# Kernel optimization log

Measured on AMD Instinct MI355X. Metric: run time of the kernel, lower is better.

Reference implementation:

```python
import jax, jax.numpy as jnp
from jax import lax
import numpy as np

B, F, H, W, D = 256, 64, 64, 64, 256  # batch, features_dim, map H, map W, input_dim
HC = 32  # hidden conv channels


def setup_inputs() -> dict:
    key = jax.random.key(0)
    ks = jax.random.split(key, 10)
    s = 0.02
    return {
        "x": jax.random.normal(ks[0], (B, D), jnp.float32),
        "state": jax.random.normal(ks[1], (B, F, H, W), jnp.float32),
        "index": jax.random.randint(ks[2], (B, 2), 0, H),
        "conv1_w": jax.random.normal(ks[3], (HC, F, 3, 3), jnp.float32) * s,
        "conv1_b": jnp.zeros((HC,), jnp.float32),
        "conv2_w": jax.random.normal(ks[4], (HC, HC, 3, 3), jnp.float32) * s,
        "conv2_b": jnp.zeros((HC,), jnp.float32),
        "conv3_w": jax.random.normal(ks[5], (HC, HC, 3, 3), jnp.float32) * s,
        "conv3_b": jnp.zeros((HC,), jnp.float32),
        "lin_w": jax.random.normal(ks[6], (HC * H * W, F), jnp.float32) * s,
        "lin_b": jnp.zeros((F,), jnp.float32),
        "write_w": jax.random.normal(ks[7], (D + 2 * F, F), jnp.float32) * s,
        "write_b": jnp.zeros((F,), jnp.float32),
    }


def _conv_relu(h, w, b):
    y = lax.conv_general_dilated(h, w, (1, 1), "SAME",
                                 dimension_numbers=("NCHW", "OIHW", "NCHW"))
    return jax.nn.relu(y + b[None, :, None, None])


def reference(x, state, index, conv1_w, conv1_b, conv2_w, conv2_b,
              conv3_w, conv3_b, lin_w, lin_b, write_w, write_b):
    h = _conv_relu(state, conv1_w, conv1_b)
    h = _conv_relu(h, conv2_w, conv2_b)
    h = _conv_relu(h, conv3_w, conv3_b)
    r = jax.nn.relu(h.reshape(B, -1) @ lin_w + lin_b)  # [B, F]
    # write: gather per-batch map cell, single Linear (MLP with no hidden layers)
    bidx = jnp.arange(B)
    m = state[bidx, :, index[:, 0], index[:, 1]]  # [B, F] gather
    w = jnp.concatenate([x, r, m], axis=1) @ write_w + write_b  # [B, F]
    # scatter updated feature vector back into the state map
    new_state = state.at[bidx, :, index[:, 0], index[:, 1]].set(w)
    return jnp.concatenate([r, w], axis=1), new_state
```

## Files before the change

kernel.cpp:

```cpp
#include <hip/hip_runtime.h>
#include <hip/hip_bf16.h>


typedef __attribute__((ext_vector_type(8))) short bf16x8;
typedef __attribute__((ext_vector_type(4))) float f32x4;

__device__ inline unsigned short f2bfu(float f) {
    __hip_bfloat16 h = __float2bfloat16(f);
    return *reinterpret_cast<unsigned short*>(&h);
}

__global__ __launch_bounds__(256)
void repack_w_k(const float* __restrict__ w1, const float* __restrict__ w2,
                const float* __restrict__ w3, __hip_bfloat16* __restrict__ rw)
{
    int idx = blockIdx.x * 256 + threadIdx.x;
    const float* src; int CIN, li;
    if (idx < 18432)      { src = w1; CIN = 64; li = idx; }
    else if (idx < 27648) { src = w2; CIN = 32; li = idx - 18432; }
    else                  { src = w3; CIN = 32; li = idx - 27648; }
    int ci = li & 31;
    int co = (li >> 5) & 31;
    int t2 = li >> 10;
    int ks = t2 % 9;
    int ch = t2 / 9;
    rw[idx] = __float2bfloat16(src[((size_t)(co * CIN + ch * 32 + ci)) * 9 + ks]);
}

template<int CIN, typename TIN>
__global__ __launch_bounds__(256, 2)
void conv_mfma_k(const TIN* __restrict__ in,
                 const __hip_bfloat16* __restrict__ rw,
                 const float* __restrict__ bias,
                 __hip_bfloat16* __restrict__ out)
{
    constexpr int NCH = CIN / 32;
    __shared__ __hip_bfloat16 s_in[18 * 34 * 40];

    const int b    = blockIdx.x;
    const int ty0  = (blockIdx.y >> 1) * 16;
    const int tx0  = (blockIdx.y & 1) * 32;
    const int t    = threadIdx.x;
    const int lane = t & 63;
    const int wv   = t >> 6;
    const int ln   = lane & 15;
    const int lg   = lane >> 4;

    const f32x4 zero4 = {0.f, 0.f, 0.f, 0.f};
    f32x4 acc[8][2];
    #pragma unroll
    for (int p = 0; p < 8; ++p) { acc[p][0] = zero4; acc[p][1] = zero4; }

    int bbase[8];
    #pragma unroll
    for (int p = 0; p < 8; ++p) {
        int gg = wv * 8 + p;
        bbase[p] = (((gg >> 1) * 34) + (gg & 1) * 16 + ln) * 80 + lg * 16;
    }

    for (int ch = 0; ch < NCH; ++ch) {
        bf16x8 wf[9][2];
        #pragma unroll
        for (int ks = 0; ks < 9; ++ks)
            #pragma unroll
            for (int cg = 0; cg < 2; ++cg)
                wf[ks][cg] = *(const bf16x8*)(rw + ((size_t)((ch * 9 + ks) * 32 + cg * 16 + ln)) * 32 + lg * 8);

        if constexpr (sizeof(TIN) == 4) {
            for (int idx = t; idx < 32 * 18 * 34; idx += 256) {
                int lx = idx % 34;
                int r  = idx / 34;
                int ly = r % 18;
                int ci = r / 18;
                int gy = ty0 - 1 + ly, gx = tx0 - 1 + lx;
                float v = 0.f;
                if ((unsigned)gy < 64u && (unsigned)gx < 64u)
                    v = in[(((size_t)b * CIN + ch * 32 + ci) * 64 + gy) * 64 + gx];
                s_in[(ly * 34 + lx) * 40 + ci] = __float2bfloat16(v);
            }
        } else {
            for (int idx = t; idx < 18 * 34 * 4; idx += 256) {
                int c8 = idx & 3, px = idx >> 2;
                int ly = px / 34, lx = px - ly * 34;
                int gy = ty0 - 1 + ly, gx = tx0 - 1 + lx;
                uint4 v = make_uint4(0u, 0u, 0u, 0u);
                if ((unsigned)gy < 64u && (unsigned)gx < 64u)
                    v = *(const uint4*)(in + ((size_t)b * 4096 + gy * 64 + gx) * 32 + c8 * 8);
                *(uint4*)(reinterpret_cast<char*>(s_in) + px * 80 + c8 * 16) = v;
            }
        }
        __syncthreads();

        #pragma unroll
        for (int ky = 0; ky < 3; ++ky)
        #pragma unroll
        for (int kx = 0; kx < 3; ++kx) {
            const int ks   = ky * 3 + kx;
            const int koff = (ky * 34 + kx) * 80;
            #pragma unroll
            for (int p = 0; p < 8; ++p) {
                bf16x8 bfr = *(const bf16x8*)(reinterpret_cast<const char*>(s_in) + bbase[p] + koff);
                acc[p][0] = __builtin_amdgcn_mfma_f32_16x16x32_bf16(wf[ks][0], bfr, acc[p][0], 0, 0, 0);
                acc[p][1] = __builtin_amdgcn_mfma_f32_16x16x32_bf16(wf[ks][1], bfr, acc[p][1], 0, 0, 0);
            }
        }
        __syncthreads();
    }

    #pragma unroll
    for (int p = 0; p < 8; ++p) {
        int gg = wv * 8 + p;
        int y  = ty0 + (gg >> 1);
        int x  = tx0 + (gg & 1) * 16 + ln;
        size_t pxb = ((size_t)b * 4096 + y * 64 + x) * 32;
        #pragma unroll
        for (int cg = 0; cg < 2; ++cg) {
            int co0 = cg * 16 + lg * 4;
            float4 bv = *(const float4*)(bias + co0);
            ushort4 o;
            o.x = f2bfu(fmaxf(acc[p][cg][0] + bv.x, 0.f));
            o.y = f2bfu(fmaxf(acc[p][cg][1] + bv.y, 0.f));
            o.z = f2bfu(fmaxf(acc[p][cg][2] + bv.z, 0.f));
            o.w = f2bfu(fmaxf(acc[p][cg][3] + bv.w, 0.f));
            *(ushort4*)(out + pxb + co0) = o;
        }
    }
}

__global__ __launch_bounds__(256)
void lin_partial_k(const __hip_bfloat16* __restrict__ h3,
                   const float* __restrict__ lw,
                   float* __restrict__ partial)
{
    __shared__ float s_h[32][260];
    __shared__ float s_w[32][64];
    const int t  = threadIdx.x;
    const int k0 = blockIdx.x * 512;
    const int f0 = (t & 15) * 4;
    const int b0 = (t >> 4) * 16;

    float acc[16][4];
    #pragma unroll
    for (int i = 0; i < 16; ++i)
        #pragma unroll
        for (int j = 0; j < 4; ++j) acc[i][j] = 0.f;

    for (int kk = 0; kk < 512; kk += 32) {
        #pragma unroll
        for (int i = 0; i < 8; ++i) {
            int id = i * 256 + t;
            int bb = id >> 3;
            int pc = id & 7;
            ushort4 hv = *(const ushort4*)(h3 + (size_t)bb * 131072 + k0 + kk + pc * 4);
            s_h[pc * 4 + 0][bb] = __uint_as_float((unsigned)hv.x << 16);
            s_h[pc * 4 + 1][bb] = __uint_as_float((unsigned)hv.y << 16);
            s_h[pc * 4 + 2][bb] = __uint_as_float((unsigned)hv.z << 16);
            s_h[pc * 4 + 3][bb] = __uint_as_float((unsigned)hv.w << 16);
        }
        #pragma unroll
        for (int i = 0; i < 2; ++i) {
            int id = i * 256 + t;
            int kr = id >> 4;
            int c4 = (id & 15) * 4;
            int k  = k0 + kk + kr;
            size_t ref = (size_t)(k & 31) * 4096 + (size_t)(k >> 5);
            float4 wv = *(const float4*)&lw[ref * 64 + c4];
            *(float4*)&s_w[kr][c4] = wv;
        }
        __syncthreads();
        for (int k = 0; k < 32; ++k) {
            float4 wv = *(const float4*)&s_w[k][f0];
            #pragma unroll
            for (int ii = 0; ii < 4; ++ii) {
                float4 hv = *(const float4*)&s_h[k][b0 + ii * 4];
                float hvv[4] = {hv.x, hv.y, hv.z, hv.w};
                #pragma unroll
                for (int l = 0; l < 4; ++l) {
                    acc[ii * 4 + l][0] += hvv[l] * wv.x;
                    acc[ii * 4 + l][1] += hvv[l] * wv.y;
                    acc[ii * 4 + l][2] += hvv[l] * wv.z;
                    acc[ii * 4 + l][3] += hvv[l] * wv.w;
                }
            }
        }
        __syncthreads();
    }

    float* pp = partial + (size_t)blockIdx.x * 16384;
    #pragma unroll
    for (int i = 0; i < 16; ++i) {
        float4 v = make_float4(acc[i][0], acc[i][1], acc[i][2], acc[i][3]);
        *(float4*)&pp[(b0 + i) * 64 + f0] = v;
    }
}

__global__ __launch_bounds__(256)
void lin_reduce_k(const float* __restrict__ partial,
                  const float* __restrict__ lb,
                  float* __restrict__ out)
{
    int idx = blockIdx.x * 256 + threadIdx.x;
    int b = idx >> 6, f = idx & 63;
    float s = lb[f];
    for (int c = 0; c < 256; ++c) s += partial[(size_t)c * 16384 + idx];
    out[(size_t)b * 128 + f] = fmaxf(s, 0.f);
}

__global__ __launch_bounds__(256)
void write_k(const float* __restrict__ x,
             const float* __restrict__ state,
             const int* __restrict__ index,
             const float* __restrict__ ww,
             const float* __restrict__ wb,
             float* __restrict__ out)
{
    int idx = blockIdx.x * 256 + threadIdx.x;
    int b = idx >> 6, f = idx & 63;
    int i0 = index[b * 2 + 0];
    int i1 = index[b * 2 + 1];
    float s = wb[f];
    for (int k = 0; k < 256; ++k) s += x[(size_t)b * 256 + k] * ww[k * 64 + f];
    for (int k = 0; k < 64; ++k)  s += out[(size_t)b * 128 + k] * ww[(256 + k) * 64 + f];
    const float* mp = state + (size_t)b * 262144 + (size_t)i0 * 64 + i1;
    for (int k = 0; k < 64; ++k)  s += mp[(size_t)k * 4096] * ww[(320 + k) * 64 + f];
    out[(size_t)b * 128 + 64 + f] = s;
}

__global__ __launch_bounds__(256)
void copy_state_k(const float4* __restrict__ src, float4* __restrict__ dst, int n4)
{
    int stride = gridDim.x * blockDim.x;
    for (int i = blockIdx.x * blockDim.x + threadIdx.x; i < n4; i += stride)
        dst[i] = src[i];
}

__global__ __launch_bounds__(256)
void scatter_k(const int* __restrict__ index,
               const float* __restrict__ out_ro,
               float* __restrict__ ns)
{
    int idx = blockIdx.x * 256 + threadIdx.x;
    int b = idx >> 6, f = idx & 63;
    int i0 = index[b * 2 + 0];
    int i1 = index[b * 2 + 1];
    ns[(((size_t)b * 64 + f) * 64 + i0) * 64 + i1] = out_ro[(size_t)b * 128 + 64 + f];
}

extern "C" void kernel_launch(void* const* d_in, const int* in_sizes, int n_in,
                              void* d_out, int out_size, void* d_ws, size_t ws_size,
                              hipStream_t stream)
{
    (void)in_sizes; (void)n_in; (void)out_size; (void)d_ws; (void)ws_size;
    const float* x     = (const float*)d_in[0];
    const float* state = (const float*)d_in[1];
    const int*   idx   = (const int*)d_in[2];
    const float* c1w   = (const float*)d_in[3];
    const float* c1b   = (const float*)d_in[4];
    const float* c2w   = (const float*)d_in[5];
    const float* c2b   = (const float*)d_in[6];
    const float* c3w   = (const float*)d_in[7];
    const float* c3b   = (const float*)d_in[8];
    const float* lw    = (const float*)d_in[9];
    const float* lb    = (const float*)d_in[10];
    const float* ww    = (const float*)d_in[11];
    const float* wb    = (const float*)d_in[12];

    float* out = (float*)d_out;
    float* ns  = out + 32768;

    __hip_bfloat16* rw  = (__hip_bfloat16*)out;
    __hip_bfloat16* rw1 = rw;
    __hip_bfloat16* rw2 = rw + 18432;
    __hip_bfloat16* rw3 = rw + 27648;

    __hip_bfloat16* h1 = (__hip_bfloat16*)ns;
    __hip_bfloat16* h2 = h1 + 33554432;
    __hip_bfloat16* h3 = h1;
    float* partial     = (float*)h2;

    repack_w_k<<<144, 256, 0, stream>>>(c1w, c2w, c3w, rw);
    conv_mfma_k<64, float>         <<<dim3(256, 8), 256, 0, stream>>>(state, rw1, c1b, h1);
    conv_mfma_k<32, __hip_bfloat16><<<dim3(256, 8), 256, 0, stream>>>(h1, rw2, c2b, h2);
    conv_mfma_k<32, __hip_bfloat16><<<dim3(256, 8), 256, 0, stream>>>(h2, rw3, c3b, h3);
    lin_partial_k<<<256, 256, 0, stream>>>(h3, lw, partial);
    lin_reduce_k <<<64, 256, 0, stream>>>(partial, lb, out);
    write_k      <<<64, 256, 0, stream>>>(x, state, idx, ww, wb, out);
    copy_state_k <<<8192, 256, 0, stream>>>((const float4*)state, (float4*)ns, 16777216);
    scatter_k    <<<64, 256, 0, stream>>>(idx, out, ns);
}
```

Baseline: 956.2 us.

## Pre-transpose state to NHWC bf16 and batch global loads in conv tiles

Adds a transpose kernel that turns the fp32 NCHW state into bf16 NHWC in scratch, so the first conv layer reuses the vectorized NHWC tile loader instead of strided per-element fp32 loads. The tile loader now issues all global loads into registers before writing shared memory, exposing more memory-level parallelism. The occupancy hint is raised to 3 blocks per CU. This costs an extra pass over the state tensor, plus added register pressure from the staged loads.

```diff
diff --git a/kernel.cpp b/kernel.cpp
--- a/kernel.cpp
+++ b/kernel.cpp
@@ -27,9 +27,38 @@
     rw[idx] = __float2bfloat16(src[((size_t)(co * CIN + ch * 32 + ci)) * 9 + ks]);
 }
 
-template<int CIN, typename TIN>
-__global__ __launch_bounds__(256, 2)
-void conv_mfma_k(const TIN* __restrict__ in,
+__global__ __launch_bounds__(256)
+void nchw_to_nhwc_k(const float* __restrict__ in,
+                    __hip_bfloat16* __restrict__ outp)
+{
+    __shared__ unsigned short s[64][72];
+    const int blk = blockIdx.x;
+    const int b = blk >> 6, y = blk & 63;
+    const int t = threadIdx.x;
+
+    const float* src = in + (size_t)b * 262144 + (size_t)y * 64;
+    #pragma unroll
+    for (int q = 0; q < 4; ++q) {
+        int c = q * 16 + (t >> 4);
+        int x = (t & 15) * 4;
+        float4 v = *(const float4*)(src + (size_t)c * 4096 + x);
+        *(ushort4*)&s[c][x] = make_ushort4(f2bfu(v.x), f2bfu(v.y), f2bfu(v.z), f2bfu(v.w));
+    }
+    __syncthreads();
+
+    __hip_bfloat16* dst = outp + ((size_t)b * 4096 + y * 64) * 64;
+    #pragma unroll
+    for (int q = 0; q < 4; ++q) {
+        int x = q * 16 + (t >> 4);
+        int c = (t & 15) * 4;
+        ushort4 o = make_ushort4(s[c + 0][x], s[c + 1][x], s[c + 2][x], s[c + 3][x]);
+        *(ushort4*)(dst + (size_t)x * 64 + c) = o;
+    }
+}
+
+template<int CIN>
+__global__ __launch_bounds__(256, 3)
+void conv_mfma_k(const __hip_bfloat16* __restrict__ in,
                  const __hip_bfloat16* __restrict__ rw,
                  const float* __restrict__ bias,
                  __hip_bfloat16* __restrict__ out)
@@ -66,27 +95,26 @@
             for (int cg = 0; cg < 2; ++cg)
                 wf[ks][cg] = *(const bf16x8*)(rw + ((size_t)((ch * 9 + ks) * 32 + cg * 16 + ln)) * 32 + lg * 8);
 
-        if constexpr (sizeof(TIN) == 4) {
-            for (int idx = t; idx < 32 * 18 * 34; idx += 256) {
-                int lx = idx % 34;
-                int r  = idx / 34;
-                int ly = r % 18;
-                int ci = r / 18;
-                int gy = ty0 - 1 + ly, gx = tx0 - 1 + lx;
-                float v = 0.f;
-                if ((unsigned)gy < 64u && (unsigned)gx < 64u)
-                    v = in[(((size_t)b * CIN + ch * 32 + ci) * 64 + gy) * 64 + gx];
-                s_in[(ly * 34 + lx) * 40 + ci] = __float2bfloat16(v);
-            }
-        } else {
-            for (int idx = t; idx < 18 * 34 * 4; idx += 256) {
-                int c8 = idx & 3, px = idx >> 2;
+        uint4 vreg[10];
+        #pragma unroll
+        for (int q = 0; q < 10; ++q) {
+            int id = q * 256 + t;
+            uint4 v = make_uint4(0u, 0u, 0u, 0u);
+            if (id < 2448) {
+                int c8 = id & 3, px = id >> 2;
                 int ly = px / 34, lx = px - ly * 34;
                 int gy = ty0 - 1 + ly, gx = tx0 - 1 + lx;
-                uint4 v = make_uint4(0u, 0u, 0u, 0u);
                 if ((unsigned)gy < 64u && (unsigned)gx < 64u)
-                    v = *(const uint4*)(in + ((size_t)b * 4096 + gy * 64 + gx) * 32 + c8 * 8);
-                *(uint4*)(reinterpret_cast<char*>(s_in) + px * 80 + c8 * 16) = v;
+                    v = *(const uint4*)(in + ((size_t)b * 4096 + gy * 64 + gx) * CIN + ch * 32 + c8 * 8);
+            }
+            vreg[q] = v;
+        }
+        #pragma unroll
+        for (int q = 0; q < 10; ++q) {
+            int id = q * 256 + t;
+            if (id < 2448) {
+                int c8 = id & 3, px = id >> 2;
+                *(uint4*)(reinterpret_cast<char*>(s_in) + px * 80 + c8 * 16) = vreg[q];
             }
         }
         __syncthreads();
@@ -273,15 +301,17 @@
     __hip_bfloat16* rw2 = rw + 18432;
     __hip_bfloat16* rw3 = rw + 27648;
 
-    __hip_bfloat16* h1 = (__hip_bfloat16*)ns;
-    __hip_bfloat16* h2 = h1 + 33554432;
-    __hip_bfloat16* h3 = h1;
-    float* partial     = (float*)h2;
-
-    repack_w_k<<<144, 256, 0, stream>>>(c1w, c2w, c3w, rw);
-    conv_mfma_k<64, float>         <<<dim3(256, 8), 256, 0, stream>>>(state, rw1, c1b, h1);
-    conv_mfma_k<32, __hip_bfloat16><<<dim3(256, 8), 256, 0, stream>>>(h1, rw2, c2b, h2);
-    conv_mfma_k<32, __hip_bfloat16><<<dim3(256, 8), 256, 0, stream>>>(h2, rw3, c3b, h3);
+    __hip_bfloat16* h1    = (__hip_bfloat16*)ns;
+    __hip_bfloat16* h2    = h1 + 33554432;
+    __hip_bfloat16* h3    = h1;
+    __hip_bfloat16* snhwc = (__hip_bfloat16*)(ns + 33554432);
+    float* partial        = (float*)h2;
+
+    repack_w_k    <<<144, 256, 0, stream>>>(c1w, c2w, c3w, rw);
+    nchw_to_nhwc_k<<<16384, 256, 0, stream>>>(state, snhwc);
+    conv_mfma_k<64><<<dim3(256, 8), 256, 0, stream>>>(snhwc, rw1, c1b, h1);
+    conv_mfma_k<32><<<dim3(256, 8), 256, 0, stream>>>(h1, rw2, c2b, h2);
+    conv_mfma_k<32><<<dim3(256, 8), 256, 0, stream>>>(h2, rw3, c3b, h3);
     lin_partial_k<<<256, 256, 0, stream>>>(h3, lw, partial);
     lin_reduce_k <<<64, 256, 0, stream>>>(partial, lb, out);
     write_k      <<<64, 256, 0, stream>>>(x, state, idx, ww, wb, out);
```

Result: faster. 846.2 us (-11.5%).
